# Kernel tuning notes

Hardware: AMD Instinct MI355X
Metric: run time of the kernel (lower is better)

## Reference

```python
import jax, jax.numpy as jnp
import numpy as np

STEEPNESS = 10.0
EPS = 1e-12

def _l2norm(x):
    return x / jnp.sqrt(jnp.sum(x * x, axis=-1, keepdims=True) + EPS)

def setup_inputs() -> dict:
    key = jax.random.key(0)
    k1, k2, k3 = jax.random.split(key, 3)
    B, D, C = 65536, 512, 1024
    return {
        "query": jax.random.normal(k1, (B, D), dtype=jnp.float32),
        "key_mem": jax.random.normal(k2, (C, D), dtype=jnp.float32),
        "val_mem": jax.random.normal(k3, (C, C), dtype=jnp.float32),
    }

def reference(query, key_mem, val_mem):
    # F.normalize(query_vectors, dim=-1)
    q = _l2norm(query)                      # (B, D)
    # cosine_similarity_multi(q, key_mem, rep='real'):
    # F.linear(F.normalize(a), F.normalize(b)) -> (B, C)
    k = _l2norm(key_mem)                    # (C, D)
    sim = jnp.einsum('bd,cd->bc', q, k)     # (B, C)
    # softabs sharpening: sigmoid(s*(x-0.5)) + sigmoid(s*(-x-0.5))
    s = STEEPNESS
    sharp = jax.nn.sigmoid(s * sim - 0.5 * s) + jax.nn.sigmoid(-s * sim - 0.5 * s)
    # normalize_weightings
    w = sharp / jnp.sum(sharp, axis=1, keepdims=True)
    # weighted value readout
    out = jnp.matmul(w, val_mem)            # (B, C)
    return out
```

## Files before the change

### kernel.cpp

```cpp
#include <hip/hip_runtime.h>
#include <hip/hip_bf16.h>

typedef __attribute__((ext_vector_type(8))) short bf16x8;
typedef __attribute__((ext_vector_type(8))) unsigned short ushort8;
typedef __attribute__((ext_vector_type(4))) float f32x4;
typedef unsigned int u32;

#define D_DIM 512
#define C_DIM 1024
#define B_DIM 65536

__device__ __forceinline__ unsigned short f2bf(float x) {
  u32 u = __float_as_uint(x);
  u32 r = (u + 0x7fffu + ((u >> 16) & 1u)) >> 16;
  return (unsigned short)r;
}

__device__ __forceinline__ void async16(const void* g, void* l) {
  __builtin_amdgcn_global_load_lds(
      (const __attribute__((address_space(1))) u32*)g,
      (__attribute__((address_space(3))) u32*)l, 16, 0, 0);
}

__device__ __forceinline__ float sharpf(float x) {
  float t = __expf(10.f * x - 5.f);
  float u = 22026.4658f * t * t;
  float num = u + 2.f * t + 1.f;
  float den = u + 22027.4658f * t + 1.f;
  return num * __builtin_amdgcn_rcpf(den);
}

__global__ __launch_bounds__(256) void rownorm_kernel(
    const float* __restrict__ src, unsigned short* __restrict__ dst) {
  int row = blockIdx.x * 4 + (threadIdx.x >> 6);
  int lane = threadIdx.x & 63;
  const float* s = src + (size_t)row * D_DIM + lane * 8;
  float4 v0 = *(const float4*)s;
  float4 v1 = *(const float4*)(s + 4);
  float ss = v0.x * v0.x + v0.y * v0.y + v0.z * v0.z + v0.w * v0.w +
             v1.x * v1.x + v1.y * v1.y + v1.z * v1.z + v1.w * v1.w;
#pragma unroll
  for (int m = 32; m >= 1; m >>= 1) ss += __shfl_xor(ss, m);
  float rinv = rsqrtf(ss + 1e-12f);
  float tv[8] = {v0.x, v0.y, v0.z, v0.w, v1.x, v1.y, v1.z, v1.w};
  ushort8 o;
#pragma unroll
  for (int i = 0; i < 8; ++i) o[i] = f2bf(tv[i] * rinv);
  *(ushort8*)(dst + (size_t)row * D_DIM + lane * 8) = o;
}

__global__ __launch_bounds__(256) void valT_kernel(
    const float* __restrict__ val, unsigned short* __restrict__ vbT) {
  __shared__ float tile[32][33];
  int bx = blockIdx.x & 31;
  int by = blockIdx.x >> 5;
  int t = threadIdx.x;
  int r = t >> 5, c = t & 31;
#pragma unroll
  for (int i = 0; i < 4; ++i)
    tile[r + i * 8][c] = val[(size_t)(by * 32 + r + i * 8) * C_DIM + bx * 32 + c];
  __syncthreads();
#pragma unroll
  for (int i = 0; i < 4; ++i)
    vbT[(size_t)(bx * 32 + r + i * 8) * C_DIM + by * 32 + c] = f2bf(tile[c][r + i * 8]);
}

__global__ __launch_bounds__(256) void rsum_reduce_kernel(
    const float* __restrict__ part, float* __restrict__ rsum) {
  int i = blockIdx.x * 256 + threadIdx.x;
  rsum[i] = (part[i] + part[i + B_DIM]) +
            (part[i + 2 * B_DIM] + part[i + 3 * B_DIM]);
}

template <int K, bool SHARP>
__global__ __launch_bounds__(512, 2) void gemm256_kernel(
    const unsigned short* __restrict__ A, const unsigned short* __restrict__ Bm,
    unsigned short* __restrict__ wout, float* __restrict__ rsum,
    float* __restrict__ fout) {
  __shared__ unsigned short smem[65536];
  const int NKT = K / 64;
  const int bid = blockIdx.x;
  const int wg = (bid & 7) * 128 + (bid >> 3);
  const int m0 = (wg >> 2) * 256;
  const int n0 = (wg & 3) * 256;
  const int t = threadIdx.x;
  const int lane = t & 63;
  const int wv = t >> 6;
  const int wr = wv >> 2;
  const int wc = wv & 3;
  const int lo = lane & 15, hi = lane >> 4;
  const int swu = (lo & 7) << 3;

  const int s_ridx = t >> 3;
  const int s_c = (t & 7) * 8;
  auto stage = [&](int T, int k) {
    int r = (s_ridx < 32) ? (k * 32 + s_ridx) : (96 + k * 32 + s_ridx);
    int cl = s_c ^ ((r & 7) << 3);
    size_t go = (size_t)T * 64 + cl;
    int d = (T & 1) * 32768;
    async16(A + (size_t)(m0 + r) * K + go, &smem[d + r * 64 + s_c]);
    async16(Bm + (size_t)(n0 + r) * K + go, &smem[d + 16384 + r * 64 + s_c]);
  };

  f32x4 acc[8][4];
#pragma unroll
  for (int i = 0; i < 8; ++i)
#pragma unroll
    for (int j = 0; j < 4; ++j) acc[i][j] = (f32x4){0.f, 0.f, 0.f, 0.f};

  stage(0, 0); stage(0, 1); stage(0, 2); stage(0, 3);
  stage(1, 0); stage(1, 1); stage(1, 2);

#pragma unroll 1
  for (int T = 0; T < NKT; ++T) {
    if (T == NKT - 1) {
      asm volatile("s_waitcnt vmcnt(0)" ::: "memory");
    } else {
      asm volatile("s_waitcnt vmcnt(6)" ::: "memory");
    }
    __builtin_amdgcn_s_barrier();
    const int d = (T & 1) * 32768;
    bf16x8 bfr[4][2];
    {
      bf16x8 af[2][2];
#pragma unroll
      for (int mi = 0; mi < 2; ++mi)
#pragma unroll
        for (int ks = 0; ks < 2; ++ks) {
          int r = wr * 128 + mi * 16 + lo;
          af[mi][ks] = *(const bf16x8*)&smem[d + r * 64 + ((ks * 32 + hi * 8) ^ swu)];
        }
#pragma unroll
      for (int nf = 0; nf < 4; ++nf)
#pragma unroll
        for (int ks = 0; ks < 2; ++ks) {
          int r = wc * 64 + nf * 16 + lo;
          bfr[nf][ks] =
              *(const bf16x8*)&smem[d + 16384 + r * 64 + ((ks * 32 + hi * 8) ^ swu)];
        }
      if (T + 1 < NKT) stage(T + 1, 3);
      __builtin_amdgcn_s_setprio(1);
#pragma unroll
      for (int mi = 0; mi < 2; ++mi)
#pragma unroll
        for (int nf = 0; nf < 4; ++nf)
#pragma unroll
          for (int ks = 0; ks < 2; ++ks)
            acc[mi][nf] = __builtin_amdgcn_mfma_f32_16x16x32_bf16(
                af[mi][ks], bfr[nf][ks], acc[mi][nf], 0, 0, 0);
      __builtin_amdgcn_s_setprio(0);
    }
#pragma unroll
    for (int p = 1; p < 4; ++p) {
      bf16x8 af[2][2];
#pragma unroll
      for (int mi = 0; mi < 2; ++mi)
#pragma unroll
        for (int ks = 0; ks < 2; ++ks) {
          int r = wr * 128 + (p * 2 + mi) * 16 + lo;
          af[mi][ks] = *(const bf16x8*)&smem[d + r * 64 + ((ks * 32 + hi * 8) ^ swu)];
        }
      __builtin_amdgcn_s_barrier();
      if (T + 2 < NKT) stage(T + 2, p - 1);
      __builtin_amdgcn_s_setprio(1);
#pragma unroll
      for (int mi = 0; mi < 2; ++mi)
#pragma unroll
        for (int nf = 0; nf < 4; ++nf)
#pragma unroll
          for (int ks = 0; ks < 2; ++ks)
            acc[p * 2 + mi][nf] = __builtin_amdgcn_mfma_f32_16x16x32_bf16(
                af[mi][ks], bfr[nf][ks], acc[p * 2 + mi][nf], 0, 0, 0);
      __builtin_amdgcn_s_setprio(0);
    }
  }
  __syncthreads();

  if (SHARP) {
    float rs[8][4];
#pragma unroll
    for (int i = 0; i < 8; ++i)
#pragma unroll
      for (int j = 0; j < 4; ++j) rs[i][j] = 0.f;
    unsigned short* ep = smem;
#pragma unroll
    for (int mf = 0; mf < 8; ++mf)
#pragma unroll
      for (int nf = 0; nf < 4; ++nf)
#pragma unroll
        for (int j = 0; j < 4; ++j) {
          float s = sharpf(acc[mf][nf][j]);
          rs[mf][j] += s;
          int rl = wr * 128 + mf * 16 + (hi << 2) + j;
          int cl = (wc * 64 + nf * 16 + lo) ^ (((rl >> 2) & 3) << 4);
          ep[rl * 256 + cl] = f2bf(s);
        }
#pragma unroll
    for (int mf = 0; mf < 8; ++mf)
#pragma unroll
      for (int j = 0; j < 4; ++j) {
        float v = rs[mf][j];
        v += __shfl_xor(v, 1);
        v += __shfl_xor(v, 2);
        v += __shfl_xor(v, 4);
        v += __shfl_xor(v, 8);
        rs[mf][j] = v;
      }
    __syncthreads();
#pragma unroll
    for (int pass = 0; pass < 16; ++pass) {
      int idx = pass * 4096 + t * 8;
      int row = idx >> 8, col = idx & 255;
      int phys = row * 256 + (col ^ (((row >> 2) & 3) << 4));
      *(ushort8*)&wout[(size_t)(m0 + row) * C_DIM + n0 + col] =
          *(const ushort8*)&ep[phys];
    }
    __syncthreads();
    float* rbuf = (float*)smem;
    if (lo == 0) {
#pragma unroll
      for (int mf = 0; mf < 8; ++mf)
#pragma unroll
        for (int j = 0; j < 4; ++j)
          rbuf[wc * 256 + wr * 128 + mf * 16 + (hi << 2) + j] = rs[mf][j];
    }
    __syncthreads();
    if (t < 256) {
      float v = (rbuf[t] + rbuf[256 + t]) + (rbuf[512 + t] + rbuf[768 + t]);
      rsum[(size_t)(wg & 3) * B_DIM + m0 + t] = v;
    }
  } else {
    float rinv[8][4];
#pragma unroll
    for (int mf = 0; mf < 8; ++mf)
#pragma unroll
      for (int j = 0; j < 4; ++j)
        rinv[mf][j] =
            __builtin_amdgcn_rcpf(rsum[m0 + wr * 128 + mf * 16 + (hi << 2) + j]);
#pragma unroll
    for (int mf = 0; mf < 8; ++mf)
#pragma unroll
      for (int nf = 0; nf < 4; ++nf)
#pragma unroll
        for (int j = 0; j < 4; ++j)
          fout[(size_t)(m0 + wr * 128 + mf * 16 + (hi << 2) + j) * C_DIM +
               n0 + wc * 64 + nf * 16 + lo] = acc[mf][nf][j] * rinv[mf][j];
  }
}

extern "C" void kernel_launch(void* const* d_in, const int* in_sizes, int n_in,
                              void* d_out, int out_size, void* d_ws, size_t ws_size,
                              hipStream_t stream) {
  const float* query = (const float*)d_in[0];
  const float* key = (const float*)d_in[1];
  const float* val = (const float*)d_in[2];
  float* out = (float*)d_out;
  const int B = in_sizes[0] / D_DIM;

  char* ws = (char*)d_ws;
  unsigned short* kb = (unsigned short*)(ws);
  unsigned short* vbT = (unsigned short*)(ws + (1ull << 20));
  float* rsum_part = (float*)(ws + 3ull * (1ull << 20));
  unsigned short* qb = (unsigned short*)(ws + 4ull * (1ull << 20));
  float* rsum = (float*)qb;
  unsigned short* wbf = (unsigned short*)(ws + 68ull * (1ull << 20));

  rownorm_kernel<<<dim3(B / 4), dim3(256), 0, stream>>>(query, qb);
  rownorm_kernel<<<dim3(C_DIM / 4), dim3(256), 0, stream>>>(key, kb);
  valT_kernel<<<dim3(1024), dim3(256), 0, stream>>>(val, vbT);

  dim3 grid((B / 256) * (C_DIM / 256));
  gemm256_kernel<D_DIM, true><<<grid, dim3(512), 0, stream>>>(qb, kb, wbf, rsum_part, nullptr);
  rsum_reduce_kernel<<<dim3(B / 256), dim3(256), 0, stream>>>(rsum_part, rsum);
  gemm256_kernel<C_DIM, false><<<grid, dim3(512), 0, stream>>>(wbf, vbT, nullptr, rsum, out);
}
```

Baseline: 326.1 us.

## Store intermediates in MFMA fragment-packed layout and load directly in second GEMM

The first GEMM epilogue and the value transpose kernel now write their bf16 outputs pre-packed in per-16-row, per-32-k fragment blocks that match the MFMA operand layout. The second GEMM drops LDS staging and async copies and loads fragments straight from global memory into registers, with the rsum read vectorised. This removes LDS traffic and barriers in the K=1024 GEMM. In exchange it gives up explicit double-buffered prefetch, so load latency now depends on occupancy and cache hits, and tile reuse across waves relies on L2 rather than shared memory.

New measurement: 357.4 us. 1.1x slower.

```diff
diff --git a/kernel.cpp b/kernel.cpp
--- a/kernel.cpp
+++ b/kernel.cpp
@@ -49,8 +49,8 @@
   *(ushort8*)(dst + (size_t)row * D_DIM + lane * 8) = o;
 }
 
-__global__ __launch_bounds__(256) void valT_kernel(
-    const float* __restrict__ val, unsigned short* __restrict__ vbT) {
+__global__ __launch_bounds__(256) void valTp_kernel(
+    const float* __restrict__ val, unsigned short* __restrict__ vp) {
   __shared__ float tile[32][33];
   int bx = blockIdx.x & 31;
   int by = blockIdx.x >> 5;
@@ -60,9 +60,17 @@
   for (int i = 0; i < 4; ++i)
     tile[r + i * 8][c] = val[(size_t)(by * 32 + r + i * 8) * C_DIM + bx * 32 + c];
   __syncthreads();
-#pragma unroll
-  for (int i = 0; i < 4; ++i)
-    vbT[(size_t)(bx * 32 + r + i * 8) * C_DIM + by * 32 + c] = f2bf(tile[c][r + i * 8]);
+  if (t < 128) {
+    int ntl = t >> 6;
+    int l = t & 63;
+    int nloc = ntl * 16 + (l & 15);
+    int k0 = (l >> 4) * 8;
+    ushort8 o;
+#pragma unroll
+    for (int e = 0; e < 8; ++e) o[e] = f2bf(tile[k0 + e][nloc]);
+    size_t nt = bx * 2 + ntl;
+    *(ushort8*)&vp[(nt * 32 + by) * 512 + (size_t)l * 8] = o;
+  }
 }
 
 __global__ __launch_bounds__(256) void rsum_reduce_kernel(
@@ -72,13 +80,11 @@
             (part[i + 2 * B_DIM] + part[i + 3 * B_DIM]);
 }
 
-template <int K, bool SHARP>
-__global__ __launch_bounds__(512, 2) void gemm256_kernel(
+__global__ __launch_bounds__(512, 2) void gemm1_kernel(
     const unsigned short* __restrict__ A, const unsigned short* __restrict__ Bm,
-    unsigned short* __restrict__ wout, float* __restrict__ rsum,
-    float* __restrict__ fout) {
+    unsigned short* __restrict__ wp, float* __restrict__ rsum) {
   __shared__ unsigned short smem[65536];
-  const int NKT = K / 64;
+  const int NKT = D_DIM / 64;
   const int bid = blockIdx.x;
   const int wg = (bid & 7) * 128 + (bid >> 3);
   const int m0 = (wg >> 2) * 256;
@@ -98,8 +104,8 @@
     int cl = s_c ^ ((r & 7) << 3);
     size_t go = (size_t)T * 64 + cl;
     int d = (T & 1) * 32768;
-    async16(A + (size_t)(m0 + r) * K + go, &smem[d + r * 64 + s_c]);
-    async16(Bm + (size_t)(n0 + r) * K + go, &smem[d + 16384 + r * 64 + s_c]);
+    async16(A + (size_t)(m0 + r) * D_DIM + go, &smem[d + r * 64 + s_c]);
+    async16(Bm + (size_t)(n0 + r) * D_DIM + go, &smem[d + 16384 + r * 64 + s_c]);
   };
 
   f32x4 acc[8][4];
@@ -176,76 +182,144 @@
   }
   __syncthreads();
 
-  if (SHARP) {
-    float rs[8][4];
-#pragma unroll
-    for (int i = 0; i < 8; ++i)
-#pragma unroll
-      for (int j = 0; j < 4; ++j) rs[i][j] = 0.f;
-    unsigned short* ep = smem;
+  float rs[8][4];
+#pragma unroll
+  for (int i = 0; i < 8; ++i)
+#pragma unroll
+    for (int j = 0; j < 4; ++j) rs[i][j] = 0.f;
+  unsigned short* ep = smem;
+#pragma unroll
+  for (int mf = 0; mf < 8; ++mf)
+#pragma unroll
+    for (int nf = 0; nf < 4; ++nf)
+#pragma unroll
+      for (int j = 0; j < 4; ++j) {
+        float s = sharpf(acc[mf][nf][j]);
+        rs[mf][j] += s;
+        int rl = wr * 128 + mf * 16 + (hi << 2) + j;
+        int cl = (wc * 64 + nf * 16 + lo) ^ ((rl & 15) << 4);
+        ep[rl * 256 + cl] = f2bf(s);
+      }
+#pragma unroll
+  for (int mf = 0; mf < 8; ++mf)
+#pragma unroll
+    for (int j = 0; j < 4; ++j) {
+      float v = rs[mf][j];
+      v += __shfl_xor(v, 1);
+      v += __shfl_xor(v, 2);
+      v += __shfl_xor(v, 4);
+      v += __shfl_xor(v, 8);
+      rs[mf][j] = v;
+    }
+  __syncthreads();
+#pragma unroll
+  for (int mt = 0; mt < 16; ++mt) {
+    int prow = mt * 16 + (lane & 15);
+    int pcol = (wv * 32 + hi * 8) ^ ((lane & 15) << 4);
+    ushort8 v = *(const ushort8*)&ep[prow * 256 + pcol];
+    size_t off = (((size_t)(m0 >> 4) + mt) * 32 + (n0 >> 5) + wv) * 512 +
+                 (size_t)lane * 8;
+    *(ushort8*)&wp[off] = v;
+  }
+  __syncthreads();
+  float* rbuf = (float*)smem;
+  if (lo == 0) {
 #pragma unroll
     for (int mf = 0; mf < 8; ++mf)
 #pragma unroll
+      for (int j = 0; j < 4; ++j)
+        rbuf[wc * 256 + wr * 128 + mf * 16 + (hi << 2) + j] = rs[mf][j];
+  }
+  __syncthreads();
+  if (t < 256) {
+    float v = (rbuf[t] + rbuf[256 + t]) + (rbuf[512 + t] + rbuf[768 + t]);
+    rsum[(size_t)(wg & 3) * B_DIM + m0 + t] = v;
+  }
+}
+
+__global__ __launch_bounds__(512, 2) void gemm2_kernel(
+    const unsigned short* __restrict__ wp, const unsigned short* __restrict__ vp,
+    const float* __restrict__ rsum, float* __restrict__ fout) {
+  const int bid = blockIdx.x;
+  const int wg = (bid & 7) * 128 + (bid >> 3);
+  const int m0 = (wg >> 2) * 256;
+  const int n0 = (wg & 3) * 256;
+  const int t = threadIdx.x;
+  const int lane = t & 63;
+  const int wv = t >> 6;
+  const int wr = wv >> 2;
+  const int wc = wv & 3;
+  const int lo = lane & 15, hi = lane >> 4;
+
+  f32x4 acc[8][4];
+#pragma unroll
+  for (int i = 0; i < 8; ++i)
+#pragma unroll
+    for (int j = 0; j < 4; ++j) acc[i][j] = (f32x4){0.f, 0.f, 0.f, 0.f};
+
+  const unsigned short* pa =
+      wp + (((size_t)(m0 >> 4) + wr * 8) * 32) * 512 + (size_t)lane * 8;
+  const unsigned short* pb =
+      vp + (((size_t)(n0 >> 4) + wc * 4) * 32) * 512 + (size_t)lane * 8;
+
+#pragma unroll 1
+  for (int T = 0; T < 16; ++T) {
+    bf16x8 af[4][2], bfr[4][2];
+#pragma unroll
+    for (int mf = 0; mf < 4; ++mf)
+#pragma unroll
+      for (int ks = 0; ks < 2; ++ks)
+        af[mf][ks] = *(const bf16x8*)(pa + ((size_t)mf * 32 + T * 2 + ks) * 512);
+#pragma unroll
+    for (int nf = 0; nf < 4; ++nf)
+#pragma unroll
+      for (int ks = 0; ks < 2; ++ks)
+        bfr[nf][ks] = *(const bf16x8*)(pb + ((size_t)nf * 32 + T * 2 + ks) * 512);
+    __builtin_amdgcn_s_setprio(1);
+#pragma unroll
+    for (int mf = 0; mf < 4; ++mf)
+#pragma unroll
       for (int nf = 0; nf < 4; ++nf)
 #pragma unroll
-        for (int j = 0; j < 4; ++j) {
-          float s = sharpf(acc[mf][nf][j]);
-          rs[mf][j] += s;
-          int rl = wr * 128 + mf * 16 + (hi << 2) + j;
-          int cl = (wc * 64 + nf * 16 + lo) ^ (((rl >> 2) & 3) << 4);
-          ep[rl * 256 + cl] = f2bf(s);
-        }
-#pragma unroll
-    for (int mf = 0; mf < 8; ++mf)
-#pragma unroll
-      for (int j = 0; j < 4; ++j) {
-        float v = rs[mf][j];
-        v += __shfl_xor(v, 1);
-        v += __shfl_xor(v, 2);
-        v += __shfl_xor(v, 4);
-        v += __shfl_xor(v, 8);
-        rs[mf][j] = v;
-      }
-    __syncthreads();
-#pragma unroll
-    for (int pass = 0; pass < 16; ++pass) {
-      int idx = pass * 4096 + t * 8;
-      int row = idx >> 8, col = idx & 255;
-      int phys = row * 256 + (col ^ (((row >> 2) & 3) << 4));
-      *(ushort8*)&wout[(size_t)(m0 + row) * C_DIM + n0 + col] =
-          *(const ushort8*)&ep[phys];
-    }
-    __syncthreads();
-    float* rbuf = (float*)smem;
-    if (lo == 0) {
-#pragma unroll
-      for (int mf = 0; mf < 8; ++mf)
-#pragma unroll
-        for (int j = 0; j < 4; ++j)
-          rbuf[wc * 256 + wr * 128 + mf * 16 + (hi << 2) + j] = rs[mf][j];
-    }
-    __syncthreads();
-    if (t < 256) {
-      float v = (rbuf[t] + rbuf[256 + t]) + (rbuf[512 + t] + rbuf[768 + t]);
-      rsum[(size_t)(wg & 3) * B_DIM + m0 + t] = v;
-    }
-  } else {
-    float rinv[8][4];
-#pragma unroll
-    for (int mf = 0; mf < 8; ++mf)
+        for (int ks = 0; ks < 2; ++ks)
+          acc[mf][nf] = __builtin_amdgcn_mfma_f32_16x16x32_bf16(
+              af[mf][ks], bfr[nf][ks], acc[mf][nf], 0, 0, 0);
+    __builtin_amdgcn_s_setprio(0);
+#pragma unroll
+    for (int mf = 0; mf < 4; ++mf)
+#pragma unroll
+      for (int ks = 0; ks < 2; ++ks)
+        af[mf][ks] =
+            *(const bf16x8*)(pa + ((size_t)(mf + 4) * 32 + T * 2 + ks) * 512);
+    __builtin_amdgcn_s_setprio(1);
+#pragma unroll
+    for (int mf = 0; mf < 4; ++mf)
+#pragma unroll
+      for (int nf = 0; nf < 4; ++nf)
+#pragma unroll
+        for (int ks = 0; ks < 2; ++ks)
+          acc[4 + mf][nf] = __builtin_amdgcn_mfma_f32_16x16x32_bf16(
+              af[mf][ks], bfr[nf][ks], acc[4 + mf][nf], 0, 0, 0);
+    __builtin_amdgcn_s_setprio(0);
+  }
+
+  float rinv[8][4];
+#pragma unroll
+  for (int mf = 0; mf < 8; ++mf) {
+    float4 r4 = *(const float4*)&rsum[m0 + wr * 128 + mf * 16 + (hi << 2)];
+    rinv[mf][0] = __builtin_amdgcn_rcpf(r4.x);
+    rinv[mf][1] = __builtin_amdgcn_rcpf(r4.y);
+    rinv[mf][2] = __builtin_amdgcn_rcpf(r4.z);
+    rinv[mf][3] = __builtin_amdgcn_rcpf(r4.w);
+  }
+#pragma unroll
+  for (int mf = 0; mf < 8; ++mf)
+#pragma unroll
+    for (int nf = 0; nf < 4; ++nf)
 #pragma unroll
       for (int j = 0; j < 4; ++j)
-        rinv[mf][j] =
-            __builtin_amdgcn_rcpf(rsum[m0 + wr * 128 + mf * 16 + (hi << 2) + j]);
-#pragma unroll
-    for (int mf = 0; mf < 8; ++mf)
-#pragma unroll
-      for (int nf = 0; nf < 4; ++nf)
-#pragma unroll
-        for (int j = 0; j < 4; ++j)
-          fout[(size_t)(m0 + wr * 128 + mf * 16 + (hi << 2) + j) * C_DIM +
-               n0 + wc * 64 + nf * 16 + lo] = acc[mf][nf][j] * rinv[mf][j];
-  }
+        fout[(size_t)(m0 + wr * 128 + mf * 16 + (hi << 2) + j) * C_DIM +
+             n0 + wc * 64 + nf * 16 + lo] = acc[mf][nf][j] * rinv[mf][j];
 }
 
 extern "C" void kernel_launch(void* const* d_in, const int* in_sizes, int n_in,
@@ -259,18 +333,18 @@
 
   char* ws = (char*)d_ws;
   unsigned short* kb = (unsigned short*)(ws);
-  unsigned short* vbT = (unsigned short*)(ws + (1ull << 20));
+  unsigned short* vp = (unsigned short*)(ws + (1ull << 20));
   float* rsum_part = (float*)(ws + 3ull * (1ull << 20));
   unsigned short* qb = (unsigned short*)(ws + 4ull * (1ull << 20));
   float* rsum = (float*)qb;
-  unsigned short* wbf = (unsigned short*)(ws + 68ull * (1ull << 20));
+  unsigned short* wp = (unsigned short*)(ws + 68ull * (1ull << 20));
 
   rownorm_kernel<<<dim3(B / 4), dim3(256), 0, stream>>>(query, qb);
   rownorm_kernel<<<dim3(C_DIM / 4), dim3(256), 0, stream>>>(key, kb);
-  valT_kernel<<<dim3(1024), dim3(256), 0, stream>>>(val, vbT);
+  valTp_kernel<<<dim3(1024), dim3(256), 0, stream>>>(val, vp);
 
   dim3 grid((B / 256) * (C_DIM / 256));
-  gemm256_kernel<D_DIM, true><<<grid, dim3(512), 0, stream>>>(qb, kb, wbf, rsum_part, nullptr);
+  gemm1_kernel<<<grid, dim3(512), 0, stream>>>(qb, kb, wp, rsum_part);
   rsum_reduce_kernel<<<dim3(B / 256), dim3(256), 0, stream>>>(rsum_part, rsum);
-  gemm256_kernel<C_DIM, false><<<grid, dim3(512), 0, stream>>>(wbf, vbT, nullptr, rsum, out);
-}
+  gemm2_kernel<<<grid, dim3(512), 0, stream>>>(wp, vp, rsum, out);
+}
```

## Merge prep kernels, fold rsum reduce into GEMM2, retile GEMM2 to 256x128

Applied to the files above, without the earlier changes.

The three preprocessing kernels (query and key row-normalisation and the value transpose) become one launch that dispatches on block index. The separate row-sum reduce kernel is removed, and the second GEMM now reads the four partial sums directly in its epilogue. GEMM2 gets its own kernel with 256x128 tiles, 256 threads, K-steps of 32 and a smaller split-stage double-buffered LDS pipeline, aiming at better occupancy and fewer launches. The trade-off is less operand reuse per tile and more global reads of A.

Result: slower. 351.0 us (+7.6%).

```diff
diff --git a/kernel.cpp b/kernel.cpp
--- a/kernel.cpp
+++ b/kernel.cpp
@@ -30,55 +30,53 @@
   return num * __builtin_amdgcn_rcpf(den);
 }
 
-__global__ __launch_bounds__(256) void rownorm_kernel(
-    const float* __restrict__ src, unsigned short* __restrict__ dst) {
-  int row = blockIdx.x * 4 + (threadIdx.x >> 6);
-  int lane = threadIdx.x & 63;
-  const float* s = src + (size_t)row * D_DIM + lane * 8;
-  float4 v0 = *(const float4*)s;
-  float4 v1 = *(const float4*)(s + 4);
-  float ss = v0.x * v0.x + v0.y * v0.y + v0.z * v0.z + v0.w * v0.w +
-             v1.x * v1.x + v1.y * v1.y + v1.z * v1.z + v1.w * v1.w;
-#pragma unroll
-  for (int m = 32; m >= 1; m >>= 1) ss += __shfl_xor(ss, m);
-  float rinv = rsqrtf(ss + 1e-12f);
-  float tv[8] = {v0.x, v0.y, v0.z, v0.w, v1.x, v1.y, v1.z, v1.w};
-  ushort8 o;
-#pragma unroll
-  for (int i = 0; i < 8; ++i) o[i] = f2bf(tv[i] * rinv);
-  *(ushort8*)(dst + (size_t)row * D_DIM + lane * 8) = o;
-}
-
-__global__ __launch_bounds__(256) void valT_kernel(
-    const float* __restrict__ val, unsigned short* __restrict__ vbT) {
+__global__ __launch_bounds__(256) void prep_kernel(
+    const float* __restrict__ q, const float* __restrict__ k,
+    const float* __restrict__ val, unsigned short* __restrict__ qb,
+    unsigned short* __restrict__ kb, unsigned short* __restrict__ vbT) {
   __shared__ float tile[32][33];
-  int bx = blockIdx.x & 31;
-  int by = blockIdx.x >> 5;
-  int t = threadIdx.x;
-  int r = t >> 5, c = t & 31;
-#pragma unroll
-  for (int i = 0; i < 4; ++i)
-    tile[r + i * 8][c] = val[(size_t)(by * 32 + r + i * 8) * C_DIM + bx * 32 + c];
-  __syncthreads();
-#pragma unroll
-  for (int i = 0; i < 4; ++i)
-    vbT[(size_t)(bx * 32 + r + i * 8) * C_DIM + by * 32 + c] = f2bf(tile[c][r + i * 8]);
-}
-
-__global__ __launch_bounds__(256) void rsum_reduce_kernel(
-    const float* __restrict__ part, float* __restrict__ rsum) {
-  int i = blockIdx.x * 256 + threadIdx.x;
-  rsum[i] = (part[i] + part[i + B_DIM]) +
-            (part[i + 2 * B_DIM] + part[i + 3 * B_DIM]);
-}
-
-template <int K, bool SHARP>
-__global__ __launch_bounds__(512, 2) void gemm256_kernel(
+  int bid = blockIdx.x;
+  if (bid < 16640) {
+    const float* src = (bid < 16384) ? q : k;
+    unsigned short* dst = (bid < 16384) ? qb : kb;
+    int b = (bid < 16384) ? bid : bid - 16384;
+    int row = b * 4 + (threadIdx.x >> 6);
+    int lane = threadIdx.x & 63;
+    const float* s = src + (size_t)row * D_DIM + lane * 8;
+    float4 v0 = *(const float4*)s;
+    float4 v1 = *(const float4*)(s + 4);
+    float ss = v0.x * v0.x + v0.y * v0.y + v0.z * v0.z + v0.w * v0.w +
+               v1.x * v1.x + v1.y * v1.y + v1.z * v1.z + v1.w * v1.w;
+#pragma unroll
+    for (int m = 32; m >= 1; m >>= 1) ss += __shfl_xor(ss, m);
+    float rinv = rsqrtf(ss + 1e-12f);
+    float tv[8] = {v0.x, v0.y, v0.z, v0.w, v1.x, v1.y, v1.z, v1.w};
+    ushort8 o;
+#pragma unroll
+    for (int i = 0; i < 8; ++i) o[i] = f2bf(tv[i] * rinv);
+    *(ushort8*)(dst + (size_t)row * D_DIM + lane * 8) = o;
+  } else {
+    int b = bid - 16640;
+    int bx = b & 31;
+    int by = b >> 5;
+    int t = threadIdx.x;
+    int r = t >> 5, c = t & 31;
+#pragma unroll
+    for (int i = 0; i < 4; ++i)
+      tile[r + i * 8][c] = val[(size_t)(by * 32 + r + i * 8) * C_DIM + bx * 32 + c];
+    __syncthreads();
+#pragma unroll
+    for (int i = 0; i < 4; ++i)
+      vbT[(size_t)(bx * 32 + r + i * 8) * C_DIM + by * 32 + c] =
+          f2bf(tile[c][r + i * 8]);
+  }
+}
+
+__global__ __launch_bounds__(512, 2) void gemm1_kernel(
     const unsigned short* __restrict__ A, const unsigned short* __restrict__ Bm,
-    unsigned short* __restrict__ wout, float* __restrict__ rsum,
-    float* __restrict__ fout) {
+    unsigned short* __restrict__ wout, float* __restrict__ rsum) {
   __shared__ unsigned short smem[65536];
-  const int NKT = K / 64;
+  const int NKT = D_DIM / 64;
   const int bid = blockIdx.x;
   const int wg = (bid & 7) * 128 + (bid >> 3);
   const int m0 = (wg >> 2) * 256;
@@ -98,8 +96,8 @@
     int cl = s_c ^ ((r & 7) << 3);
     size_t go = (size_t)T * 64 + cl;
     int d = (T & 1) * 32768;
-    async16(A + (size_t)(m0 + r) * K + go, &smem[d + r * 64 + s_c]);
-    async16(Bm + (size_t)(n0 + r) * K + go, &smem[d + 16384 + r * 64 + s_c]);
+    async16(A + (size_t)(m0 + r) * D_DIM + go, &smem[d + r * 64 + s_c]);
+    async16(Bm + (size_t)(n0 + r) * D_DIM + go, &smem[d + 16384 + r * 64 + s_c]);
   };
 
   f32x4 acc[8][4];
@@ -176,76 +174,194 @@
   }
   __syncthreads();
 
-  if (SHARP) {
-    float rs[8][4];
-#pragma unroll
-    for (int i = 0; i < 8; ++i)
-#pragma unroll
-      for (int j = 0; j < 4; ++j) rs[i][j] = 0.f;
-    unsigned short* ep = smem;
+  float rs[8][4];
+#pragma unroll
+  for (int i = 0; i < 8; ++i)
+#pragma unroll
+    for (int j = 0; j < 4; ++j) rs[i][j] = 0.f;
+  unsigned short* ep = smem;
+#pragma unroll
+  for (int mf = 0; mf < 8; ++mf)
+#pragma unroll
+    for (int nf = 0; nf < 4; ++nf)
+#pragma unroll
+      for (int j = 0; j < 4; ++j) {
+        float s = sharpf(acc[mf][nf][j]);
+        rs[mf][j] += s;
+        int rl = wr * 128 + mf * 16 + (hi << 2) + j;
+        int cl = (wc * 64 + nf * 16 + lo) ^ (((rl >> 2) & 3) << 4);
+        ep[rl * 256 + cl] = f2bf(s);
+      }
+#pragma unroll
+  for (int mf = 0; mf < 8; ++mf)
+#pragma unroll
+    for (int j = 0; j < 4; ++j) {
+      float v = rs[mf][j];
+      v += __shfl_xor(v, 1);
+      v += __shfl_xor(v, 2);
+      v += __shfl_xor(v, 4);
+      v += __shfl_xor(v, 8);
+      rs[mf][j] = v;
+    }
+  __syncthreads();
+#pragma unroll
+  for (int pass = 0; pass < 16; ++pass) {
+    int idx = pass * 4096 + t * 8;
+    int row = idx >> 8, col = idx & 255;
+    int phys = row * 256 + (col ^ (((row >> 2) & 3) << 4));
+    *(ushort8*)&wout[(size_t)(m0 + row) * C_DIM + n0 + col] =
+        *(const ushort8*)&ep[phys];
+  }
+  __syncthreads();
+  float* rbuf = (float*)smem;
+  if (lo == 0) {
 #pragma unroll
     for (int mf = 0; mf < 8; ++mf)
 #pragma unroll
-      for (int nf = 0; nf < 4; ++nf)
-#pragma unroll
-        for (int j = 0; j < 4; ++j) {
-          float s = sharpf(acc[mf][nf][j]);
-          rs[mf][j] += s;
-          int rl = wr * 128 + mf * 16 + (hi << 2) + j;
-          int cl = (wc * 64 + nf * 16 + lo) ^ (((rl >> 2) & 3) << 4);
-          ep[rl * 256 + cl] = f2bf(s);
-        }
-#pragma unroll
-    for (int mf = 0; mf < 8; ++mf)
-#pragma unroll
-      for (int j = 0; j < 4; ++j) {
-        float v = rs[mf][j];
-        v += __shfl_xor(v, 1);
-        v += __shfl_xor(v, 2);
-        v += __shfl_xor(v, 4);
-        v += __shfl_xor(v, 8);
-        rs[mf][j] = v;
+      for (int j = 0; j < 4; ++j)
+        rbuf[wc * 256 + wr * 128 + mf * 16 + (hi << 2) + j] = rs[mf][j];
+  }
+  __syncthreads();
+  if (t < 256) {
+    float v = (rbuf[t] + rbuf[256 + t]) + (rbuf[512 + t] + rbuf[768 + t]);
+    rsum[(size_t)(wg & 3) * B_DIM + m0 + t] = v;
+  }
+}
+
+__global__ __launch_bounds__(256, 2) void gemm2_kernel(
+    const unsigned short* __restrict__ A, const unsigned short* __restrict__ Bm,
+    const float* __restrict__ part, float* __restrict__ fout) {
+  __shared__ unsigned short smem[24576];
+  const int NKT = C_DIM / 32;
+  const int bid = blockIdx.x;
+  const int wg = (bid & 7) * 256 + (bid >> 3);
+  const int m0 = (wg >> 3) * 256;
+  const int n0 = (wg & 7) * 128;
+  const int t = threadIdx.x;
+  const int lane = t & 63;
+  const int wv = t >> 6;
+  const int wr = wv >> 1;
+  const int wc = wv & 1;
+  const int lo = lane & 15, hi = lane >> 4;
+
+  auto stage_b1 = [&](int T) {
+    const int d = (T & 1) * 12288;
+#pragma unroll
+    for (int i = 0; i < 2; ++i) {
+      int s = i * 256 + t;
+      int rl = s >> 2;
+      int r = 64 + (rl & 63) + (rl >> 6) * 128;
+      int sc = (s & 3) * 8;
+      int cl = sc ^ ((r & 3) << 3);
+      async16(A + (size_t)(m0 + r) * C_DIM + (size_t)T * 32 + cl,
+              &smem[d + r * 32 + sc]);
+    }
+  };
+  auto stage_b0B = [&](int T) {
+    const int d = (T & 1) * 12288;
+#pragma unroll
+    for (int i = 0; i < 2; ++i) {
+      int s = i * 256 + t;
+      int rl = s >> 2;
+      int r = (rl & 63) + (rl >> 6) * 128;
+      int sc = (s & 3) * 8;
+      int cl = sc ^ ((r & 3) << 3);
+      async16(A + (size_t)(m0 + r) * C_DIM + (size_t)T * 32 + cl,
+              &smem[d + r * 32 + sc]);
+    }
+#pragma unroll
+    for (int i = 0; i < 2; ++i) {
+      int s = i * 256 + t;
+      int n = s >> 2;
+      int sc = (s & 3) * 8;
+      int cl = sc ^ ((n & 3) << 3);
+      async16(Bm + (size_t)(n0 + n) * C_DIM + (size_t)T * 32 + cl,
+              &smem[d + 8192 + n * 32 + sc]);
+    }
+  };
+
+  f32x4 acc[8][4];
+#pragma unroll
+  for (int i = 0; i < 8; ++i)
+#pragma unroll
+    for (int j = 0; j < 4; ++j) acc[i][j] = (f32x4){0.f, 0.f, 0.f, 0.f};
+
+  stage_b0B(0); stage_b1(0); stage_b0B(1);
+
+#pragma unroll 1
+  for (int T = 0; T < NKT; ++T) {
+    if (T == NKT - 1) {
+      asm volatile("s_waitcnt vmcnt(0)" ::: "memory");
+    } else {
+      asm volatile("s_waitcnt vmcnt(4)" ::: "memory");
+    }
+    __builtin_amdgcn_s_barrier();
+    const int d = (T & 1) * 12288;
+    bf16x8 bfr[4];
+    {
+      bf16x8 af[4];
+#pragma unroll
+      for (int mf = 0; mf < 4; ++mf) {
+        int r = wr * 128 + mf * 16 + lo;
+        af[mf] = *(const bf16x8*)&smem[d + r * 32 + ((hi * 8) ^ ((r & 3) << 3))];
       }
-    __syncthreads();
-#pragma unroll
-    for (int pass = 0; pass < 16; ++pass) {
-      int idx = pass * 4096 + t * 8;
-      int row = idx >> 8, col = idx & 255;
-      int phys = row * 256 + (col ^ (((row >> 2) & 3) << 4));
-      *(ushort8*)&wout[(size_t)(m0 + row) * C_DIM + n0 + col] =
-          *(const ushort8*)&ep[phys];
-    }
-    __syncthreads();
-    float* rbuf = (float*)smem;
-    if (lo == 0) {
-#pragma unroll
-      for (int mf = 0; mf < 8; ++mf)
-#pragma unroll
-        for (int j = 0; j < 4; ++j)
-          rbuf[wc * 256 + wr * 128 + mf * 16 + (hi << 2) + j] = rs[mf][j];
-    }
-    __syncthreads();
-    if (t < 256) {
-      float v = (rbuf[t] + rbuf[256 + t]) + (rbuf[512 + t] + rbuf[768 + t]);
-      rsum[(size_t)(wg & 3) * B_DIM + m0 + t] = v;
-    }
-  } else {
-    float rinv[8][4];
-#pragma unroll
-    for (int mf = 0; mf < 8; ++mf)
+#pragma unroll
+      for (int nf = 0; nf < 4; ++nf) {
+        int n = wc * 64 + nf * 16 + lo;
+        bfr[nf] =
+            *(const bf16x8*)&smem[d + 8192 + n * 32 + ((hi * 8) ^ ((n & 3) << 3))];
+      }
+      if (T + 1 < NKT) stage_b1(T + 1);
+      __builtin_amdgcn_s_setprio(1);
+#pragma unroll
+      for (int mf = 0; mf < 4; ++mf)
+#pragma unroll
+        for (int nf = 0; nf < 4; ++nf)
+          acc[mf][nf] = __builtin_amdgcn_mfma_f32_16x16x32_bf16(
+              af[mf], bfr[nf], acc[mf][nf], 0, 0, 0);
+      __builtin_amdgcn_s_setprio(0);
+    }
+    {
+      bf16x8 af[4];
+#pragma unroll
+      for (int mf = 0; mf < 4; ++mf) {
+        int r = wr * 128 + (4 + mf) * 16 + lo;
+        af[mf] = *(const bf16x8*)&smem[d + r * 32 + ((hi * 8) ^ ((r & 3) << 3))];
+      }
+      __builtin_amdgcn_s_barrier();
+      if (T + 2 < NKT) stage_b0B(T + 2);
+      __builtin_amdgcn_s_setprio(1);
+#pragma unroll
+      for (int mf = 0; mf < 4; ++mf)
+#pragma unroll
+        for (int nf = 0; nf < 4; ++nf)
+          acc[4 + mf][nf] = __builtin_amdgcn_mfma_f32_16x16x32_bf16(
+              af[mf], bfr[nf], acc[4 + mf][nf], 0, 0, 0);
+      __builtin_amdgcn_s_setprio(0);
+    }
+  }
+
+  float rinv[8][4];
+#pragma unroll
+  for (int mf = 0; mf < 8; ++mf) {
+    int base = m0 + wr * 128 + mf * 16 + (hi << 2);
+    float4 p0 = *(const float4*)&part[base];
+    float4 p1 = *(const float4*)&part[B_DIM + base];
+    float4 p2 = *(const float4*)&part[2 * B_DIM + base];
+    float4 p3 = *(const float4*)&part[3 * B_DIM + base];
+    rinv[mf][0] = __builtin_amdgcn_rcpf((p0.x + p1.x) + (p2.x + p3.x));
+    rinv[mf][1] = __builtin_amdgcn_rcpf((p0.y + p1.y) + (p2.y + p3.y));
+    rinv[mf][2] = __builtin_amdgcn_rcpf((p0.z + p1.z) + (p2.z + p3.z));
+    rinv[mf][3] = __builtin_amdgcn_rcpf((p0.w + p1.w) + (p2.w + p3.w));
+  }
+#pragma unroll
+  for (int mf = 0; mf < 8; ++mf)
+#pragma unroll
+    for (int nf = 0; nf < 4; ++nf)
 #pragma unroll
       for (int j = 0; j < 4; ++j)
-        rinv[mf][j] =
-            __builtin_amdgcn_rcpf(rsum[m0 + wr * 128 + mf * 16 + (hi << 2) + j]);
-#pragma unroll
-    for (int mf = 0; mf < 8; ++mf)
-#pragma unroll
-      for (int nf = 0; nf < 4; ++nf)
-#pragma unroll
-        for (int j = 0; j < 4; ++j)
-          fout[(size_t)(m0 + wr * 128 + mf * 16 + (hi << 2) + j) * C_DIM +
-               n0 + wc * 64 + nf * 16 + lo] = acc[mf][nf][j] * rinv[mf][j];
-  }
+        fout[(size_t)(m0 + wr * 128 + mf * 16 + (hi << 2) + j) * C_DIM +
+             n0 + wc * 64 + nf * 16 + lo] = acc[mf][nf][j] * rinv[mf][j];
 }
 
 extern "C" void kernel_launch(void* const* d_in, const int* in_sizes, int n_in,
@@ -262,15 +378,11 @@
   unsigned short* vbT = (unsigned short*)(ws + (1ull << 20));
   float* rsum_part = (float*)(ws + 3ull * (1ull << 20));
   unsigned short* qb = (unsigned short*)(ws + 4ull * (1ull << 20));
-  float* rsum = (float*)qb;
   unsigned short* wbf = (unsigned short*)(ws + 68ull * (1ull << 20));
 
-  rownorm_kernel<<<dim3(B / 4), dim3(256), 0, stream>>>(query, qb);
-  rownorm_kernel<<<dim3(C_DIM / 4), dim3(256), 0, stream>>>(key, kb);
-  valT_kernel<<<dim3(1024), dim3(256), 0, stream>>>(val, vbT);
-
-  dim3 grid((B / 256) * (C_DIM / 256));
-  gemm256_kernel<D_DIM, true><<<grid, dim3(512), 0, stream>>>(qb, kb, wbf, rsum_part, nullptr);
-  rsum_reduce_kernel<<<dim3(B / 256), dim3(256), 0, stream>>>(rsum_part, rsum);
-  gemm256_kernel<C_DIM, false><<<grid, dim3(512), 0, stream>>>(wbf, vbT, nullptr, rsum, out);
-}
+  prep_kernel<<<dim3(17664), dim3(256), 0, stream>>>(query, key, val, qb, kb, vbT);
+  gemm1_kernel<<<dim3((B / 256) * (C_DIM / 256)), dim3(512), 0, stream>>>(
+      qb, kb, wbf, rsum_part);
+  gemm2_kernel<<<dim3((B / 256) * (C_DIM / 128)), dim3(256), 0, stream>>>(
+      wbf, vbT, rsum_part, out);
+}
```
